# Optimization experiments

Hardware: AMD Instinct MI355X
Metric: run time of the kernel (lower is better)

## Reference

```python
import jax, jax.numpy as jnp
import numpy as np

KERNEL_SIZE = 21
SIGMA = 3.0


def _gaussian_kernel_2d(kernel_size, sigma, dtype):
    ax = jnp.arange(kernel_size, dtype=dtype) - (kernel_size - 1) / 2.0
    xx, yy = jnp.meshgrid(ax, ax, indexing='ij')
    k = jnp.exp(-(xx ** 2 + yy ** 2) / (2.0 * sigma ** 2))
    return k / jnp.sum(k)


def setup_inputs() -> dict:
    key = jax.random.key(0)
    x = jax.random.normal(key, (32, 3, 512, 512), dtype=jnp.float32)
    return {"x": x}


def reference(x):
    B, C, H, W = x.shape
    k2d = _gaussian_kernel_2d(KERNEL_SIZE, SIGMA, x.dtype)  # [K, K]
    # depthwise weights: OIHW with feature_group_count=C -> [C, 1, K, K]
    w = jnp.broadcast_to(k2d[None, None], (C, 1, KERNEL_SIZE, KERNEL_SIZE))
    pad = KERNEL_SIZE // 2
    x_pad = jnp.pad(x, ((0, 0), (0, 0), (pad, pad), (pad, pad)), mode='reflect')
    y = jax.lax.conv_general_dilated(
        x_pad, w,
        window_strides=(1, 1),
        padding='VALID',
        dimension_numbers=('NCHW', 'OIHW', 'NCHW'),
        feature_group_count=C,
    )
    return y
```

## Files before the change

### kernel.cpp

```cpp
#include <hip/hip_runtime.h>

#define HH  512
#define WW  512
#define RAD 10
#define KK  21
#define SEG 16
#define NROWS (SEG + 2 * RAD)
#define LSTRIDE 540

__global__ __launch_bounds__(512, 8) void gauss_blur_kernel(
    const float* __restrict__ x, float* __restrict__ out)
{
    const float wt[KK] = {
        0.00051432f, 0.00147793f, 0.00380033f, 0.00874446f, 0.01800488f,
        0.03317359f, 0.05469399f, 0.08069227f, 0.10652936f, 0.12584957f,
        0.13303907f,
        0.12584957f, 0.10652936f, 0.08069227f, 0.05469399f, 0.03317359f,
        0.01800488f, 0.00874446f, 0.00380033f, 0.00147793f, 0.00051432f
    };

    __shared__ __align__(16) float vbuf[SEG * LSTRIDE];

    const int bid = blockIdx.y * gridDim.x + blockIdx.x;
    const int cpx = (gridDim.x * gridDim.y) >> 3;
    const int lid = (bid & 7) * cpx + (bid >> 3);
    const int y0  = (lid & 31) * SEG;
    const int img = lid >> 5;

    const int t = threadIdx.x;

    const float* xim = x   + (size_t)img * (HH * WW);
    float*       oim = out + (size_t)img * (HH * WW);

    float rows[NROWS];
    #pragma unroll
    for (int i = 0; i < NROWS; ++i) {
        int r  = y0 - RAD + i;
        int rr = r < 0 ? -r : (r > HH - 1 ? 2 * (HH - 1) - r : r);
        rows[i] = xim[rr * WW + t];
    }

    #pragma unroll
    for (int r = 0; r < SEG; ++r) {
        float v = 0.f;
        #pragma unroll
        for (int k = 0; k < KK; ++k)
            v = fmaf(wt[k], rows[r + k], v);
        float* vb = vbuf + r * LSTRIDE;
        vb[RAD + t] = v;
        if (t >= 1 && t <= RAD)                   vb[RAD - t] = v;
        if (t >= WW - 1 - RAD && t <= WW - 2)     vb[RAD + 2 * (WW - 1) - t] = v;
    }

    __syncthreads();

    const int r = t & (SEG - 1);
    const int q = t >> 4;
    const float* vr = vbuf + r * LSTRIDE + q * 16;

    float wnd[36];
    #pragma unroll
    for (int j = 0; j < 9; ++j) {
        float4 v4 = *(const float4*)(vr + 4 * j);
        wnd[4*j]   = v4.x; wnd[4*j+1] = v4.y;
        wnd[4*j+2] = v4.z; wnd[4*j+3] = v4.w;
    }

    float acc[16];
    #pragma unroll
    for (int j = 0; j < 16; ++j) {
        float s = 0.f;
        #pragma unroll
        for (int k = 0; k < KK; ++k)
            s = fmaf(wt[k], wnd[j + k], s);
        acc[j] = s;
    }

    float* op = oim + (size_t)(y0 + r) * WW + q * 16;
    #pragma unroll
    for (int j = 0; j < 4; ++j)
        *(float4*)(op + 4 * j) =
            make_float4(acc[4*j], acc[4*j+1], acc[4*j+2], acc[4*j+3]);
}

extern "C" void kernel_launch(void* const* d_in, const int* in_sizes, int n_in,
                              void* d_out, int out_size, void* d_ws, size_t ws_size,
                              hipStream_t stream) {
    const float* x = (const float*)d_in[0];
    float* out = (float*)d_out;
    const int n_img = in_sizes[0] / (HH * WW);
    dim3 grid(HH / SEG, n_img);
    gauss_blur_kernel<<<grid, dim3(512), 0, stream>>>(x, out);
}
```

Before: 183.0 us.

## Process four row segments per block, reusing halo rows in registers

Each block now covers 64 rows in four 16-row segments. Input rows are slid down in registers so only 16 new rows are loaded per segment, which removes the repeated 20-row vertical halo reads. The next segment's loads are issued before the current horizontal pass to overlap them. Both passes are rewritten in scatter (input-outer) form so each loaded value is kept live only briefly. The trade-off is a 4x smaller grid, extra syncs and a lower occupancy hint (6 blocks instead of 8).

```diff
diff --git a/kernel.cpp b/kernel.cpp
--- a/kernel.cpp
+++ b/kernel.cpp
@@ -5,10 +5,11 @@
 #define RAD 10
 #define KK  21
 #define SEG 16
+#define SEGS 4
 #define NROWS (SEG + 2 * RAD)
 #define LSTRIDE 540
 
-__global__ __launch_bounds__(512, 8) void gauss_blur_kernel(
+__global__ __launch_bounds__(512, 6) void gauss_blur_kernel(
     const float* __restrict__ x, float* __restrict__ out)
 {
     const float wt[KK] = {
@@ -24,8 +25,8 @@
     const int bid = blockIdx.y * gridDim.x + blockIdx.x;
     const int cpx = (gridDim.x * gridDim.y) >> 3;
     const int lid = (bid & 7) * cpx + (bid >> 3);
-    const int y0  = (lid & 31) * SEG;
-    const int img = lid >> 5;
+    const int y0  = (lid & 7) * (SEG * SEGS);
+    const int img = lid >> 3;
 
     const int t = threadIdx.x;
 
@@ -33,54 +34,104 @@
     float*       oim = out + (size_t)img * (HH * WW);
 
     float rows[NROWS];
+
     #pragma unroll
     for (int i = 0; i < NROWS; ++i) {
         int r  = y0 - RAD + i;
         int rr = r < 0 ? -r : (r > HH - 1 ? 2 * (HH - 1) - r : r);
         rows[i] = xim[rr * WW + t];
     }
-
+    {
+        float acc[SEG];
+        #pragma unroll
+        for (int r = 0; r < SEG; ++r) acc[r] = 0.f;
+        #pragma unroll
+        for (int i = 0; i < NROWS; ++i) {
+            const int lo = (i - 2 * RAD) < 0 ? 0 : (i - 2 * RAD);
+            const int hi = i < (SEG - 1) ? i : (SEG - 1);
+            #pragma unroll
+            for (int r = lo; r <= hi; ++r)
+                acc[r] = fmaf(wt[i - r], rows[i], acc[r]);
+        }
+        #pragma unroll
+        for (int r = 0; r < SEG; ++r) {
+            float* vb = vbuf + r * LSTRIDE;
+            vb[RAD + t] = acc[r];
+            if (t >= 1 && t <= RAD)               vb[RAD - t] = acc[r];
+            if (t >= WW - 1 - RAD && t <= WW - 2) vb[RAD + 2 * (WW - 1) - t] = acc[r];
+        }
+    }
     #pragma unroll
-    for (int r = 0; r < SEG; ++r) {
-        float v = 0.f;
-        #pragma unroll
-        for (int k = 0; k < KK; ++k)
-            v = fmaf(wt[k], rows[r + k], v);
-        float* vb = vbuf + r * LSTRIDE;
-        vb[RAD + t] = v;
-        if (t >= 1 && t <= RAD)                   vb[RAD - t] = v;
-        if (t >= WW - 1 - RAD && t <= WW - 2)     vb[RAD + 2 * (WW - 1) - t] = v;
-    }
-
+    for (int i = 0; i < NROWS - SEG; ++i) rows[i] = rows[i + SEG];
     __syncthreads();
 
-    const int r = t & (SEG - 1);
-    const int q = t >> 4;
-    const float* vr = vbuf + r * LSTRIDE + q * 16;
+    for (int s = 0; s < SEGS; ++s) {
+        if (s + 1 < SEGS) {
+            #pragma unroll
+            for (int i = 0; i < SEG; ++i) {
+                int r  = y0 + SEG * (s + 1) - RAD + (NROWS - SEG) + i;
+                int rr = r < 0 ? -r : (r > HH - 1 ? 2 * (HH - 1) - r : r);
+                rows[(NROWS - SEG) + i] = xim[rr * WW + t];
+            }
+        }
 
-    float wnd[36];
-    #pragma unroll
-    for (int j = 0; j < 9; ++j) {
-        float4 v4 = *(const float4*)(vr + 4 * j);
-        wnd[4*j]   = v4.x; wnd[4*j+1] = v4.y;
-        wnd[4*j+2] = v4.z; wnd[4*j+3] = v4.w;
+        {
+            const int r = t & (SEG - 1);
+            const int q = t >> 4;
+            const float* vr = vbuf + r * LSTRIDE + q * 16;
+
+            float acc[16];
+            #pragma unroll
+            for (int j = 0; j < 16; ++j) acc[j] = 0.f;
+
+            #pragma unroll
+            for (int j = 0; j < 9; ++j) {
+                const float4 v4 = *(const float4*)(vr + 4 * j);
+                const float va[4] = { v4.x, v4.y, v4.z, v4.w };
+                #pragma unroll
+                for (int e = 0; e < 4; ++e) {
+                    const int i  = 4 * j + e;
+                    const int lo = (i - 2 * RAD) < 0 ? 0 : (i - 2 * RAD);
+                    const int hi = i < 15 ? i : 15;
+                    #pragma unroll
+                    for (int o = lo; o <= hi; ++o)
+                        acc[o] = fmaf(wt[i - o], va[e], acc[o]);
+                }
+            }
+
+            float* op = oim + (size_t)(y0 + SEG * s + r) * WW + q * 16;
+            #pragma unroll
+            for (int j = 0; j < 4; ++j)
+                *(float4*)(op + 4 * j) =
+                    make_float4(acc[4*j], acc[4*j+1], acc[4*j+2], acc[4*j+3]);
+        }
+
+        if (s + 1 < SEGS) {
+            __syncthreads();
+
+            float acc[SEG];
+            #pragma unroll
+            for (int r = 0; r < SEG; ++r) acc[r] = 0.f;
+            #pragma unroll
+            for (int i = 0; i < NROWS; ++i) {
+                const int lo = (i - 2 * RAD) < 0 ? 0 : (i - 2 * RAD);
+                const int hi = i < (SEG - 1) ? i : (SEG - 1);
+                #pragma unroll
+                for (int r = lo; r <= hi; ++r)
+                    acc[r] = fmaf(wt[i - r], rows[i], acc[r]);
+            }
+            #pragma unroll
+            for (int r = 0; r < SEG; ++r) {
+                float* vb = vbuf + r * LSTRIDE;
+                vb[RAD + t] = acc[r];
+                if (t >= 1 && t <= RAD)               vb[RAD - t] = acc[r];
+                if (t >= WW - 1 - RAD && t <= WW - 2) vb[RAD + 2 * (WW - 1) - t] = acc[r];
+            }
+            #pragma unroll
+            for (int i = 0; i < NROWS - SEG; ++i) rows[i] = rows[i + SEG];
+            __syncthreads();
+        }
     }
-
-    float acc[16];
-    #pragma unroll
-    for (int j = 0; j < 16; ++j) {
-        float s = 0.f;
-        #pragma unroll
-        for (int k = 0; k < KK; ++k)
-            s = fmaf(wt[k], wnd[j + k], s);
-        acc[j] = s;
-    }
-
-    float* op = oim + (size_t)(y0 + r) * WW + q * 16;
-    #pragma unroll
-    for (int j = 0; j < 4; ++j)
-        *(float4*)(op + 4 * j) =
-            make_float4(acc[4*j], acc[4*j+1], acc[4*j+2], acc[4*j+3]);
 }
 
 extern "C" void kernel_launch(void* const* d_in, const int* in_sizes, int n_in,
@@ -89,6 +140,6 @@
     const float* x = (const float*)d_in[0];
     float* out = (float*)d_out;
     const int n_img = in_sizes[0] / (HH * WW);
-    dim3 grid(HH / SEG, n_img);
+    dim3 grid(HH / (SEG * SEGS), n_img);
     gauss_blur_kernel<<<grid, dim3(512), 0, stream>>>(x, out);
 }
```

Measured after the change: 202.4 us. 10.6% more time.

## Process four strips per block with LDS ring buffer and async global-to-LDS prefetch

Applied to the files above, without the earlier changes.

Each block now handles four consecutive 16-row strips instead of one. Input rows go into a 52-row LDS ring buffer through global_load_lds, so the 20-row vertical halo is reused across strips and the next strip's rows are fetched while the current one is computed. The intent is to cut redundant global reads of halo rows and hide load latency. In exchange the grid is four times smaller and LDS use is much larger (about 138 KB per block), which limits occupancy. There is also a possible race: the prefetch writes ring slots without waiting, and the first fetch overlaps row slots the current strip still reads.

```diff
diff --git a/kernel.cpp b/kernel.cpp
--- a/kernel.cpp
+++ b/kernel.cpp
@@ -1,14 +1,16 @@
 #include <hip/hip_runtime.h>
+#include <stdint.h>
 
-#define HH  512
-#define WW  512
-#define RAD 10
-#define KK  21
-#define SEG 16
-#define NROWS (SEG + 2 * RAD)
+#define HH   512
+#define WW   512
+#define RAD  10
+#define KK   21
+#define SEG  16
+#define TILES 4
+#define RING 52
 #define LSTRIDE 540
 
-__global__ __launch_bounds__(512, 8) void gauss_blur_kernel(
+__global__ __launch_bounds__(512, 2) void gauss_blur_kernel(
     const float* __restrict__ x, float* __restrict__ out)
 {
     const float wt[KK] = {
@@ -19,68 +21,121 @@
         0.01800488f, 0.00874446f, 0.00380033f, 0.00147793f, 0.00051432f
     };
 
+    __shared__ __align__(16) float raw[RING * WW];
     __shared__ __align__(16) float vbuf[SEG * LSTRIDE];
 
     const int bid = blockIdx.y * gridDim.x + blockIdx.x;
     const int cpx = (gridDim.x * gridDim.y) >> 3;
     const int lid = (bid & 7) * cpx + (bid >> 3);
-    const int y0  = (lid & 31) * SEG;
-    const int img = lid >> 5;
+    const int bs  = lid & 7;
+    const int img = lid >> 3;
 
-    const int t = threadIdx.x;
+    const int t    = threadIdx.x;
+    const int wave = t >> 6;
+    const int lane = t & 63;
 
     const float* xim = x   + (size_t)img * (HH * WW);
     float*       oim = out + (size_t)img * (HH * WW);
 
-    float rows[NROWS];
-    #pragma unroll
-    for (int i = 0; i < NROWS; ++i) {
-        int r  = y0 - RAD + i;
-        int rr = r < 0 ? -r : (r > HH - 1 ? 2 * (HH - 1) - r : r);
-        rows[i] = xim[rr * WW + t];
-    }
+    const int strip0 = bs * TILES;
 
     #pragma unroll
-    for (int r = 0; r < SEG; ++r) {
-        float v = 0.f;
-        #pragma unroll
-        for (int k = 0; k < KK; ++k)
-            v = fmaf(wt[k], rows[r + k], v);
-        float* vb = vbuf + r * LSTRIDE;
-        vb[RAD + t] = v;
-        if (t >= 1 && t <= RAD)                   vb[RAD - t] = v;
-        if (t >= WW - 1 - RAD && t <= WW - 2)     vb[RAD + 2 * (WW - 1) - t] = v;
+    for (int k = 0; k < 9; ++k) {
+        const int chunk = wave * 9 + k;
+        const int i     = chunk >> 1;
+        const int half  = chunk & 1;
+        const int r     = strip0 * SEG - RAD + i;
+        const int rr    = r < 0 ? -r : (r > HH - 1 ? 2 * (HH - 1) - r : r);
+        const int slot  = (r + RAD) % RING;
+        __builtin_amdgcn_global_load_lds(
+            (const __attribute__((address_space(1))) void*)
+                (xim + rr * WW + half * 256 + lane * 4),
+            (__attribute__((address_space(3))) void*)
+                (raw + slot * WW + half * 256),
+            16, 0, 0);
     }
-
     __syncthreads();
 
-    const int r = t & (SEG - 1);
-    const int q = t >> 4;
-    const float* vr = vbuf + r * LSTRIDE + q * 16;
+    for (int s = 0; s < TILES; ++s) {
+        const int strip = strip0 + s;
+        const int y0    = strip * SEG;
 
-    float wnd[36];
-    #pragma unroll
-    for (int j = 0; j < 9; ++j) {
-        float4 v4 = *(const float4*)(vr + 4 * j);
-        wnd[4*j]   = v4.x; wnd[4*j+1] = v4.y;
-        wnd[4*j+2] = v4.z; wnd[4*j+3] = v4.w;
+        if (s + 1 < TILES) {
+            #pragma unroll
+            for (int k = 0; k < 4; ++k) {
+                const int j    = 2 * wave + (k >> 1);
+                const int half = k & 1;
+                const int r    = y0 + 26 + j;
+                const int rr   = r > HH - 1 ? 2 * (HH - 1) - r : r;
+                const int slot = (r + RAD) % RING;
+                __builtin_amdgcn_global_load_lds(
+                    (const __attribute__((address_space(1))) void*)
+                        (xim + rr * WW + half * 256 + lane * 4),
+                    (__attribute__((address_space(3))) void*)
+                        (raw + slot * WW + half * 256),
+                    16, 0, 0);
+            }
+        }
+
+        {
+            float acc[SEG];
+            #pragma unroll
+            for (int r = 0; r < SEG; ++r) acc[r] = 0.f;
+
+            const int sb = y0 % RING;
+            #pragma unroll
+            for (int i = 0; i < 36; ++i) {
+                int slot = sb + i; if (slot >= RING) slot -= RING;
+                const float f = raw[slot * WW + t];
+                const int lo = (i - 2 * RAD) < 0 ? 0 : (i - 2 * RAD);
+                const int hi = i < (SEG - 1) ? i : (SEG - 1);
+                #pragma unroll
+                for (int r = lo; r <= hi; ++r)
+                    acc[r] = fmaf(wt[i - r], f, acc[r]);
+            }
+            #pragma unroll
+            for (int r = 0; r < SEG; ++r) {
+                float* vb = vbuf + r * LSTRIDE;
+                vb[RAD + t] = acc[r];
+                if (t >= 1 && t <= RAD)               vb[RAD - t] = acc[r];
+                if (t >= WW - 1 - RAD && t <= WW - 2) vb[RAD + 2 * (WW - 1) - t] = acc[r];
+            }
+        }
+
+        __syncthreads();
+
+        {
+            const int r = t & (SEG - 1);
+            const int q = t >> 4;
+            const float* vr = vbuf + r * LSTRIDE + q * 16;
+
+            float wnd[36];
+            #pragma unroll
+            for (int j = 0; j < 9; ++j) {
+                float4 v4 = *(const float4*)(vr + 4 * j);
+                wnd[4*j]   = v4.x; wnd[4*j+1] = v4.y;
+                wnd[4*j+2] = v4.z; wnd[4*j+3] = v4.w;
+            }
+
+            float acc[16];
+            #pragma unroll
+            for (int j = 0; j < 16; ++j) {
+                float ss = 0.f;
+                #pragma unroll
+                for (int k = 0; k < KK; ++k)
+                    ss = fmaf(wt[k], wnd[j + k], ss);
+                acc[j] = ss;
+            }
+
+            float* op = oim + (size_t)(y0 + r) * WW + q * 16;
+            #pragma unroll
+            for (int j = 0; j < 4; ++j)
+                *(float4*)(op + 4 * j) =
+                    make_float4(acc[4*j], acc[4*j+1], acc[4*j+2], acc[4*j+3]);
+        }
+
+        __syncthreads();
     }
-
-    float acc[16];
-    #pragma unroll
-    for (int j = 0; j < 16; ++j) {
-        float s = 0.f;
-        #pragma unroll
-        for (int k = 0; k < KK; ++k)
-            s = fmaf(wt[k], wnd[j + k], s);
-        acc[j] = s;
-    }
-
-    float* op = oim + (size_t)(y0 + r) * WW + q * 16;
-    #pragma unroll
-    for (int j = 0; j < 4; ++j)
-        *(float4*)(op + 4 * j) =
-            make_float4(acc[4*j], acc[4*j+1], acc[4*j+2], acc[4*j+3]);
 }
 
 extern "C" void kernel_launch(void* const* d_in, const int* in_sizes, int n_in,
@@ -89,6 +144,6 @@
     const float* x = (const float*)d_in[0];
     float* out = (float*)d_out;
     const int n_img = in_sizes[0] / (HH * WW);
-    dim3 grid(HH / SEG, n_img);
+    dim3 grid(HH / (SEG * TILES), n_img);
     gauss_blur_kernel<<<grid, dim3(512), 0, stream>>>(x, out);
 }
```

Result: slower. 209.5 us (+14.5%).
